# Optimization experiments

Measured on AMD Instinct MI355X. Metric: run time of the kernel, lower is better.

## Reference

```python
import jax, jax.numpy as jnp
import numpy as np

HEADS = 4
DIM_HEAD = 64
SCALE = 8.0
EPS = 1e-5  # fp32 branch of the original LayerNorm


def setup_inputs() -> dict:
    key = jax.random.key(0)
    k1, k2, k3 = jax.random.split(key, 3)
    B, C, F, H, W = 2, 256, 4, 32, 32
    inner = HEADS * DIM_HEAD  # 256
    x = jax.random.normal(k1, (B, C, F, H, W), dtype=jnp.float32)
    gamma = jnp.ones((1, C, 1, 1, 1), dtype=jnp.float32)
    w_qkv = jax.random.normal(k2, (3 * inner, C), dtype=jnp.float32) * 0.05
    w_out = jax.random.normal(k3, (C, inner), dtype=jnp.float32) * 0.05
    return {"x": x, "gamma": gamma, "w_qkv": w_qkv, "w_out": w_out}


def _l2norm(t):
    return t / jnp.sqrt(jnp.sum(t * t, axis=-1, keepdims=True) + 1e-12)


def reference(x, gamma, w_qkv, w_out):
    B, C, F, H, W = x.shape
    N = F * H * W
    inner = HEADS * DIM_HEAD
    residual = x

    # channel LayerNorm (biased variance over dim=1)
    mean = jnp.mean(x, axis=1, keepdims=True)
    var = jnp.mean((x - mean) ** 2, axis=1, keepdims=True)
    xn = (x - mean) / jnp.sqrt(var + EPS) * gamma

    # 1x1x1 conv == channel matmul; flatten spatial dims to sequence
    xn_flat = xn.reshape(B, C, N)                      # [B, C, N]
    qkv = jnp.einsum('oc,bcn->bon', w_qkv, xn_flat)    # [B, 3*inner, N]
    qkv = qkv.reshape(B, 3, HEADS, DIM_HEAD, N)        # chunk then split heads
    qkv = jnp.transpose(qkv, (1, 0, 2, 4, 3))          # [3, B, h, N, d]
    q, k, v = qkv[0], qkv[1], qkv[2]

    q = _l2norm(q)
    k = _l2norm(k)

    sim = jnp.einsum('bhid,bhjd->bhij', q, k) * SCALE  # [B, h, N, N]
    attn = jax.nn.softmax(sim, axis=-1)
    out = jnp.einsum('bhij,bhjd->bhid', attn, v)       # [B, h, N, d]

    # 'b h n d -> b (h d) n' then 1x1x1 out conv
    out = jnp.transpose(out, (0, 1, 3, 2)).reshape(B, inner, N)
    out = jnp.einsum('oi,bin->bon', w_out, out).reshape(B, C, F, H, W)
    return out + residual
```

## Files before the change

### kernel.cpp

```cpp
#include <hip/hip_runtime.h>

#define BATCH 2
#define CCH   256
#define NSEQ  4096
#define NH    4
#define DH    64
#define INNER 256

typedef __attribute__((ext_vector_type(8))) __bf16 bf16x8;
typedef __attribute__((ext_vector_type(4))) float f32x4;
typedef __attribute__((ext_vector_type(8))) unsigned short u16x8;
typedef __attribute__((ext_vector_type(4))) unsigned short u16x4;

#define GLD16(gsrc, ldst)                                                     \
  __builtin_amdgcn_global_load_lds(                                           \
      (const __attribute__((address_space(1))) unsigned int*)(const void*)(gsrc), \
      (__attribute__((address_space(3))) unsigned int*)(void*)(ldst), 16, 0, 0)

static __device__ __forceinline__ unsigned short f2bfr(float f) {
  union { float f; unsigned u; } v; v.f = f;
  return (unsigned short)((v.u + 0x8000u) >> 16);
}
static __device__ __forceinline__ unsigned pack2(float f0, float f1) {
  union { float f; unsigned u; } a, b; a.f = f0; b.f = f1;
  return __builtin_amdgcn_perm(b.u + 0x8000u, a.u + 0x8000u, 0x07060302u);
}
static __device__ __forceinline__ float bf2f(unsigned short u) {
  union { unsigned u; float f; } v; v.u = ((unsigned)u) << 16;
  return v.f;
}
static __device__ __forceinline__ bf16x8 ldb(const unsigned short* p) {
  return *(const bf16x8*)p;
}
static __device__ __forceinline__ f32x4 mm(bf16x8 a, bf16x8 b, f32x4 c) {
  return __builtin_amdgcn_mfma_f32_16x16x32_bf16(a, b, c, 0, 0, 0);
}
static __device__ __forceinline__ float ex2(float x) {
  return __builtin_amdgcn_exp2f(x);
}

__global__ __launch_bounds__(256) void k_lncvt(const float* __restrict__ x,
                                               const float* __restrict__ gamma,
                                               unsigned short* __restrict__ xn,
                                               const float* __restrict__ wq,
                                               const float* __restrict__ wo,
                                               unsigned short* __restrict__ wqb,
                                               unsigned short* __restrict__ wob) {
  int blk = blockIdx.x;
  if (blk >= 256) {
    int t = (blk - 256) * 256 + threadIdx.x;
    int e = t * 4;
    if (e < 768 * 256) {
      float4 v = *(const float4*)(wq + e);
      u16x4 pk = { f2bfr(v.x), f2bfr(v.y), f2bfr(v.z), f2bfr(v.w) };
      *(u16x4*)(wqb + e) = pk;
    } else {
      int e2 = e - 768 * 256;
      float4 v = *(const float4*)(wo + e2);
      u16x4 pk = { f2bfr(v.x), f2bfr(v.y), f2bfr(v.z), f2bfr(v.w) };
      *(u16x4*)(wob + e2) = pk;
    }
    return;
  }
  int b  = blk >> 7;
  int n0 = (blk & 127) * 32;
  int t  = threadIdx.x;
  int nl = t & 31;
  int cg = t >> 5;
  int n  = n0 + nl;
  const float* xp = x + ((size_t)(b * CCH + cg * 32)) * NSEQ + n;
  float vals[32];
  float s = 0.f, s2 = 0.f;
#pragma unroll
  for (int j = 0; j < 32; j++) {
    float v = xp[(size_t)j * NSEQ];
    vals[j] = v; s += v; s2 += v * v;
  }
  __shared__ float rs[8][32], rs2[8][32];
  rs[cg][nl] = s; rs2[cg][nl] = s2;
  __syncthreads();
  float S = 0.f, S2 = 0.f;
#pragma unroll
  for (int g = 0; g < 8; g++) { S += rs[g][nl]; S2 += rs2[g][nl]; }
  float mean = S * (1.f / 256.f);
  float var  = S2 * (1.f / 256.f) - mean * mean;
  float rstd = rsqrtf(var + 1e-5f);
  unsigned short* dst = xn + ((size_t)b * NSEQ + n) * CCH + cg * 32;
#pragma unroll
  for (int j0 = 0; j0 < 32; j0 += 8) {
    u16x8 pk;
#pragma unroll
    for (int j = 0; j < 8; j++)
      pk[j] = f2bfr((vals[j0 + j] - mean) * rstd * gamma[cg * 32 + j0 + j]);
    *(u16x8*)(dst + j0) = pk;
  }
}

__global__ __launch_bounds__(256) void k_qkv(const unsigned short* __restrict__ wqb,
                                             const unsigned short* __restrict__ xn,
                                             unsigned short* __restrict__ qkv,
                                             unsigned short* __restrict__ qt,
                                             unsigned short* __restrict__ ktb) {
  int n0 = blockIdx.x * 64;
  int oi = blockIdx.y;
  int o0 = oi * 64;
  int b  = blockIdx.z;
  __shared__ unsigned short Al[64 * 128];
  __shared__ unsigned short Bl[64 * 128];
  int t = threadIdx.x;
  int lane = t & 63, w = t >> 6;
  int c = lane & 15, quad = lane >> 4;
  int wm = w >> 1, wn = w & 1;
  f32x4 acc[2][2] = {};
  int lr = lane >> 4;
  int lchk = lane & 15;
  const unsigned short* apg = wqb + (size_t)o0 * CCH;
  const unsigned short* bpg = xn + ((size_t)b * NSEQ + n0) * CCH;
  for (int kt = 0; kt < 2; kt++) {
    if (kt) __syncthreads();
#pragma unroll
    for (int q = 0; q < 4; q++) {
      int r = w * 16 + q * 4 + lr;
      int srcoff = r * CCH + kt * 128 + ((lchk ^ (r & 7)) * 8);
      GLD16(apg + srcoff, Al + (size_t)(w * 16 + q * 4) * 128);
      GLD16(bpg + srcoff, Bl + (size_t)(w * 16 + q * 4) * 128);
    }
    __syncthreads();
#pragma unroll
    for (int ks = 0; ks < 4; ks++) {
      int ra0 = wm * 32 + c, ra1 = ra0 + 16;
      int rb0 = wn * 32 + c, rb1 = rb0 + 16;
      bf16x8 a0 = ldb(&Al[ra0 * 128 + (((ks * 4 + quad) ^ (ra0 & 7)) * 8)]);
      bf16x8 a1 = ldb(&Al[ra1 * 128 + (((ks * 4 + quad) ^ (ra1 & 7)) * 8)]);
      bf16x8 b0 = ldb(&Bl[rb0 * 128 + (((ks * 4 + quad) ^ (rb0 & 7)) * 8)]);
      bf16x8 b1 = ldb(&Bl[rb1 * 128 + (((ks * 4 + quad) ^ (rb1 & 7)) * 8)]);
      acc[0][0] = mm(a0, b0, acc[0][0]);
      acc[0][1] = mm(a0, b1, acc[0][1]);
      acc[1][0] = mm(a1, b0, acc[1][0]);
      acc[1][1] = mm(a1, b1, acc[1][1]);
    }
  }
  if (oi < 8) {
    float* sq = (float*)Al;
    float s0 = 0.f, s1 = 0.f;
#pragma unroll
    for (int i = 0; i < 2; i++)
#pragma unroll
      for (int rr = 0; rr < 4; rr++) {
        s0 += acc[i][0][rr] * acc[i][0][rr];
        s1 += acc[i][1][rr] * acc[i][1][rr];
      }
    s0 += __shfl_xor(s0, 16); s0 += __shfl_xor(s0, 32);
    s1 += __shfl_xor(s1, 16); s1 += __shfl_xor(s1, 32);
    __syncthreads();
    if (quad == 0) {
      sq[wm * 64 + wn * 32 + c]      = s0;
      sq[wm * 64 + wn * 32 + 16 + c] = s1;
    }
    __syncthreads();
    float r0 = rsqrtf(sq[wn * 32 + c]      + sq[64 + wn * 32 + c]      + 1e-12f);
    float r1 = rsqrtf(sq[wn * 32 + 16 + c] + sq[64 + wn * 32 + 16 + c] + 1e-12f);
    if (oi < 4) { r0 *= 11.541560327111707f; r1 *= 11.541560327111707f; }
    int h = oi & 3;
    unsigned short* base = (oi < 4 ? qt : ktb) + ((size_t)(b * NH + h) * NSEQ) * DH;
#pragma unroll
    for (int i = 0; i < 2; i++)
#pragma unroll
      for (int j = 0; j < 2; j++) {
        float rsc = j ? r1 : r0;
        int n = n0 + wn * 32 + j * 16 + c;
        int d = wm * 32 + i * 16 + quad * 4;
        uint2 pk = { pack2(acc[i][j][0] * rsc, acc[i][j][1] * rsc),
                     pack2(acc[i][j][2] * rsc, acc[i][j][3] * rsc) };
        *(uint2*)(base + (size_t)n * DH + d) = pk;
      }
  } else {
#pragma unroll
    for (int i = 0; i < 2; i++)
#pragma unroll
      for (int j = 0; j < 2; j++)
#pragma unroll
        for (int rr = 0; rr < 4; rr++) {
          int o = o0 + wm * 32 + i * 16 + quad * 4 + rr;
          int n = n0 + wn * 32 + j * 16 + c;
          qkv[((size_t)b * 768 + o) * NSEQ + n] = f2bfr(acc[i][j][rr]);
        }
  }
}

__global__ __launch_bounds__(256, 4) void k_attn(
    const unsigned short* __restrict__ qt,
    const unsigned short* __restrict__ ktb,
    const unsigned short* __restrict__ qkv,
    unsigned short* __restrict__ opart,
    float* __restrict__ lpart,
    int S, int kvlen) {
  int i0 = blockIdx.x * 128;
  int h  = blockIdx.y;
  int bz = blockIdx.z;
  int b  = bz / S, s = bz % S;
  __shared__ unsigned short Kl[64 * 64];
  __shared__ unsigned short Vl[2][64 * 64];
  __shared__ unsigned short Pl[128 * 64];
  int t = threadIdx.x;
  int lane = t & 63, w = t >> 6;
  int c = lane & 15, quad = lane >> 4;

  const unsigned short* qbase = qt  + ((size_t)(b * NH + h) * NSEQ) * DH;
  const unsigned short* kbase = ktb + ((size_t)(b * NH + h) * NSEQ) * DH;
  const unsigned short* vbase = qkv + ((size_t)b * 768 + 512 + h * 64) * NSEQ;

  int rlo = w * 32 + c, rhi = rlo + 16;
  const unsigned short* qlo = qbase + (size_t)(i0 + rlo) * DH + quad * 8;
  const unsigned short* qhi = qlo + 16 * DH;
  bf16x8 qlo0 = ldb(qlo), qlo1 = ldb(qlo + 32);
  bf16x8 qhi0 = ldb(qhi), qhi1 = ldb(qhi + 32);

  u16x8 onesu;
#pragma unroll
  for (int j = 0; j < 8; j++) onesu[j] = 0x3F80;
  bf16x8 ones = *(bf16x8*)&onesu;

  f32x4 acclo[4] = {}, acchi[4] = {};
  f32x4 accllo = {}, acclhi = {};

  int slr = lane >> 3, slc = lane & 7;
  int ssw = (slc ^ slr) * 8;
  const unsigned short* kp = kbase + (size_t)(s * kvlen + w * 16 + slr) * DH + ssw;
  const unsigned short* vp = vbase + (size_t)(w * 16 + slr) * NSEQ + s * kvlen + ssw;
  int sw0 = (quad ^ (c & 7)) * 8;
  int sw1 = sw0 ^ 32;
  int r7 = rlo & 7;

  int nIt = kvlen / 64;
  GLD16(kp,            &Kl[(w * 16)     * 64]);
  GLD16(kp + 8 * DH,   &Kl[(w * 16 + 8) * 64]);
  GLD16(vp,            &Vl[0][(w * 16)     * 64]);
  GLD16(vp + 8 * NSEQ, &Vl[0][(w * 16 + 8) * 64]);
  kp += 64 * DH; vp += 64;

  for (int it = 0; it < nIt; it++) {
    int cur = it & 1;
    __syncthreads();
    if (it + 1 < nIt) {
      int nb = cur ^ 1;
      GLD16(vp,            &Vl[nb][(w * 16)     * 64]);
      GLD16(vp + 8 * NSEQ, &Vl[nb][(w * 16 + 8) * 64]);
      vp += 64;
    }

#pragma unroll
    for (int jt = 0; jt < 4; jt++) {
      bf16x8 k0 = ldb(&Kl[(jt * 16 + c) * 64 + sw0]);
      bf16x8 k1 = ldb(&Kl[(jt * 16 + c) * 64 + sw1]);
      f32x4 zl = {}; zl = mm(k0, qlo0, zl); zl = mm(k1, qlo1, zl);
      f32x4 zh = {}; zh = mm(k0, qhi0, zh); zh = mm(k1, qhi1, zh);
      int cj = jt * 2 + (quad >> 1);
      int sub = (quad & 1) * 4;
      uint2 pkl = { pack2(ex2(zl[0]), ex2(zl[1])),
                    pack2(ex2(zl[2]), ex2(zl[3])) };
      *(uint2*)&Pl[rlo * 64 + ((cj ^ r7) * 8) + sub] = pkl;
      uint2 pkh = { pack2(ex2(zh[0]), ex2(zh[1])),
                    pack2(ex2(zh[2]), ex2(zh[3])) };
      *(uint2*)&Pl[rhi * 64 + ((cj ^ r7) * 8) + sub] = pkh;
    }
    bf16x8 plo0 = ldb(&Pl[rlo * 64 + ((quad ^ r7) * 8)]);
    bf16x8 plo1 = ldb(&Pl[rlo * 64 + (((quad + 4) ^ r7) * 8)]);
    bf16x8 phi0 = ldb(&Pl[rhi * 64 + ((quad ^ r7) * 8)]);
    bf16x8 phi1 = ldb(&Pl[rhi * 64 + (((quad + 4) ^ r7) * 8)]);

    if (it + 1 < nIt) {
      asm volatile("s_waitcnt lgkmcnt(0)" ::: "memory");
      __builtin_amdgcn_sched_barrier(0);
      __builtin_amdgcn_s_barrier();
      __builtin_amdgcn_sched_barrier(0);
      GLD16(kp,          &Kl[(w * 16)     * 64]);
      GLD16(kp + 8 * DH, &Kl[(w * 16 + 8) * 64]);
      kp += 64 * DH;
    }

#pragma unroll
    for (int dt = 0; dt < 4; dt++) {
      bf16x8 v0 = ldb(&Vl[cur][(dt * 16 + c) * 64 + sw0]);
      bf16x8 v1 = ldb(&Vl[cur][(dt * 16 + c) * 64 + sw1]);
      acclo[dt] = mm(plo0, v0, acclo[dt]);
      acclo[dt] = mm(plo1, v1, acclo[dt]);
      acchi[dt] = mm(phi0, v0, acchi[dt]);
      acchi[dt] = mm(phi1, v1, acchi[dt]);
    }
    accllo = mm(plo0, ones, accllo); accllo = mm(plo1, ones, accllo);
    acclhi = mm(phi0, ones, acclhi); acclhi = mm(phi1, ones, acclhi);
  }

  size_t rb = ((size_t)(b * NH + h) * S + s) * NSEQ + i0 + w * 32;
  if (c == 0) {
#pragma unroll
    for (int rr = 0; rr < 4; rr++) {
      lpart[rb + quad * 4 + rr]      = accllo[rr];
      lpart[rb + 16 + quad * 4 + rr] = acclhi[rr];
    }
  }
#pragma unroll
  for (int rr = 0; rr < 4; rr++)
#pragma unroll
    for (int dt = 0; dt < 4; dt++) {
      opart[(rb + quad * 4 + rr) * 64 + dt * 16 + c]      = f2bfr(acclo[dt][rr]);
      opart[(rb + 16 + quad * 4 + rr) * 64 + dt * 16 + c] = f2bfr(acchi[dt][rr]);
    }
}

__global__ __launch_bounds__(256) void k_merge(
    const unsigned short* __restrict__ opart,
    const float* __restrict__ lpart,
    unsigned short* __restrict__ ao, int S) {
  int t = blockIdx.x * 256 + threadIdx.x;
  int row = t >> 2;
  int dseg = (t & 3) * 16;
  int b = row >> 14, rem = row & 16383;
  int h = rem >> 12, i = rem & 4095;

  float l = 0.f;
  float o[16];
#pragma unroll
  for (int j = 0; j < 16; j++) o[j] = 0.f;
  for (int s = 0; s < S; s++) {
    size_t rb = ((size_t)(b * NH + h) * S + s) * NSEQ + i;
    l += lpart[rb];
    const unsigned short* p = opart + rb * 64 + dseg;
    u16x8 v0 = *(const u16x8*)p;
    u16x8 v1 = *(const u16x8*)(p + 8);
#pragma unroll
    for (int j = 0; j < 8; j++) {
      o[j]     += bf2f(v0[j]);
      o[8 + j] += bf2f(v1[j]);
    }
  }
  float inv = 1.f / l;
  unsigned short* dst = ao + ((size_t)b * NSEQ + i) * INNER + h * 64 + dseg;
  uint4 pk0 = { pack2(o[0] * inv, o[1] * inv),  pack2(o[2] * inv, o[3] * inv),
                pack2(o[4] * inv, o[5] * inv),  pack2(o[6] * inv, o[7] * inv) };
  uint4 pk1 = { pack2(o[8] * inv, o[9] * inv),  pack2(o[10] * inv, o[11] * inv),
                pack2(o[12] * inv, o[13] * inv),pack2(o[14] * inv, o[15] * inv) };
  *(uint4*)dst = pk0;
  *(uint4*)(dst + 8) = pk1;
}

__global__ __launch_bounds__(256) void k_out(const unsigned short* __restrict__ wob,
                                             const unsigned short* __restrict__ ao,
                                             const float* __restrict__ x,
                                             float* __restrict__ out) {
  int n0 = blockIdx.x * 64;
  int o0 = blockIdx.y * 64;
  int b  = blockIdx.z;
  __shared__ unsigned short Al[64 * 128];
  __shared__ unsigned short Bl[64 * 128];
  int t = threadIdx.x;
  int lane = t & 63, w = t >> 6;
  int c = lane & 15, quad = lane >> 4;
  int wm = w >> 1, wn = w & 1;
  f32x4 acc[2][2] = {};
  int lr = lane >> 4;
  int lchk = lane & 15;
  const unsigned short* apg = wob + (size_t)o0 * INNER;
  const unsigned short* bpg = ao + ((size_t)b * NSEQ + n0) * INNER;
  for (int kt = 0; kt < 2; kt++) {
    if (kt) __syncthreads();
#pragma unroll
    for (int q = 0; q < 4; q++) {
      int r = w * 16 + q * 4 + lr;
      int srcoff = r * INNER + kt * 128 + ((lchk ^ (r & 7)) * 8);
      GLD16(apg + srcoff, Al + (size_t)(w * 16 + q * 4) * 128);
      GLD16(bpg + srcoff, Bl + (size_t)(w * 16 + q * 4) * 128);
    }
    __syncthreads();
#pragma unroll
    for (int ks = 0; ks < 4; ks++) {
      int ra0 = wm * 32 + c, ra1 = ra0 + 16;
      int rb0 = wn * 32 + c, rb1 = rb0 + 16;
      bf16x8 a0 = ldb(&Al[ra0 * 128 + (((ks * 4 + quad) ^ (ra0 & 7)) * 8)]);
      bf16x8 a1 = ldb(&Al[ra1 * 128 + (((ks * 4 + quad) ^ (ra1 & 7)) * 8)]);
      bf16x8 b0 = ldb(&Bl[rb0 * 128 + (((ks * 4 + quad) ^ (rb0 & 7)) * 8)]);
      bf16x8 b1 = ldb(&Bl[rb1 * 128 + (((ks * 4 + quad) ^ (rb1 & 7)) * 8)]);
      acc[0][0] = mm(a0, b0, acc[0][0]);
      acc[0][1] = mm(a0, b1, acc[0][1]);
      acc[1][0] = mm(a1, b0, acc[1][0]);
      acc[1][1] = mm(a1, b1, acc[1][1]);
    }
  }
#pragma unroll
  for (int i = 0; i < 2; i++)
#pragma unroll
    for (int j = 0; j < 2; j++)
#pragma unroll
      for (int rr = 0; rr < 4; rr++) {
        int o = o0 + wm * 32 + i * 16 + quad * 4 + rr;
        int n = n0 + wn * 32 + j * 16 + c;
        size_t idx = ((size_t)b * CCH + o) * NSEQ + n;
        out[idx] = acc[i][j][rr] + x[idx];
      }
}

extern "C" void kernel_launch(void* const* d_in, const int* in_sizes, int n_in,
                              void* d_out, int out_size, void* d_ws, size_t ws_size,
                              hipStream_t stream) {
  const float* x     = (const float*)d_in[0];
  const float* gamma = (const float*)d_in[1];
  const float* wq    = (const float*)d_in[2];
  const float* wo    = (const float*)d_in[3];
  float* out = (float*)d_out;

  const size_t MB = 1u << 20;
  char* ws = (char*)d_ws;
  unsigned short* ao  = (unsigned short*)ws;
  unsigned short* xn  = (unsigned short*)(ws + 4 * MB);
  unsigned short* qkv = (unsigned short*)(ws + 8 * MB);
  unsigned short* wqb = (unsigned short*)(ws + 20 * MB);
  unsigned short* wob = (unsigned short*)(ws + 20 * MB + 512 * 1024);
  unsigned short* qt  = (unsigned short*)(ws + 21 * MB);
  unsigned short* ktb = (unsigned short*)(ws + 25 * MB);
  unsigned short* opart = (unsigned short*)(ws + 29 * MB);
  int S;
  if (ws_size >= 48 * MB) S = 4;
  else if (ws_size >= 40 * MB) S = 2;
  else S = 1;
  size_t opart_bytes = (size_t)S * BATCH * NH * NSEQ * DH * 2;
  float* lpart = (float*)(ws + 29 * MB + opart_bytes);
  int kvlen = NSEQ / S;

  k_lncvt<<<dim3(512),          256, 0, stream>>>(x, gamma, xn, wq, wo, wqb, wob);
  k_qkv  <<<dim3(64, 12, 2),    256, 0, stream>>>(wqb, xn, qkv, qt, ktb);
  k_attn <<<dim3(32, 4, 2 * S), 256, 0, stream>>>(qt, ktb, qkv, opart,
                                                  lpart, S, kvlen);
  k_merge<<<dim3(512),          256, 0, stream>>>(opart, lpart, ao, S);
  k_out  <<<dim3(64, 4, 2),     256, 0, stream>>>(wob, ao, x, out);
}
```

Before: 130.0 us.

## Load full K in GEMMs, use hardware bf16 pack, add setprio around MFMAs

The QKV and output projection kernels now stage the whole 256-wide reduction dimension in LDS in one pass, which removes the second load phase and its barrier at the cost of twice the LDS per block (64 KB). In the attention kernel, the manual rounding/perm bf16 packing is replaced with the v_cvt_pk_bf16_f32 instruction. MFMA groups are wrapped in s_setprio to favour matrix issue across waves. An explicit lgkmcnt(0) wait before the barrier is dropped to shorten the stall. Dropping that wait may race on LDS reuse of the K buffer, and the larger LDS footprint lowers occupancy in the GEMMs.

```diff
diff --git a/kernel.cpp b/kernel.cpp
--- a/kernel.cpp
+++ b/kernel.cpp
@@ -24,6 +24,11 @@
 static __device__ __forceinline__ unsigned pack2(float f0, float f1) {
   union { float f; unsigned u; } a, b; a.f = f0; b.f = f1;
   return __builtin_amdgcn_perm(b.u + 0x8000u, a.u + 0x8000u, 0x07060302u);
+}
+static __device__ __forceinline__ unsigned cvtpk(float lo, float hi) {
+  unsigned r;
+  asm("v_cvt_pk_bf16_f32 %0, %1, %2" : "=v"(r) : "v"(lo), "v"(hi));
+  return r;
 }
 static __device__ __forceinline__ float bf2f(unsigned short u) {
   union { unsigned u; float f; } v; v.u = ((unsigned)u) << 16;
@@ -105,40 +110,37 @@
   int oi = blockIdx.y;
   int o0 = oi * 64;
   int b  = blockIdx.z;
-  __shared__ unsigned short Al[64 * 128];
-  __shared__ unsigned short Bl[64 * 128];
+  __shared__ unsigned short Al[64 * 256];
+  __shared__ unsigned short Bl[64 * 256];
   int t = threadIdx.x;
   int lane = t & 63, w = t >> 6;
   int c = lane & 15, quad = lane >> 4;
   int wm = w >> 1, wn = w & 1;
   f32x4 acc[2][2] = {};
-  int lr = lane >> 4;
-  int lchk = lane & 15;
+  int lr2 = lane >> 5;
+  int lch = lane & 31;
   const unsigned short* apg = wqb + (size_t)o0 * CCH;
   const unsigned short* bpg = xn + ((size_t)b * NSEQ + n0) * CCH;
-  for (int kt = 0; kt < 2; kt++) {
-    if (kt) __syncthreads();
-#pragma unroll
-    for (int q = 0; q < 4; q++) {
-      int r = w * 16 + q * 4 + lr;
-      int srcoff = r * CCH + kt * 128 + ((lchk ^ (r & 7)) * 8);
-      GLD16(apg + srcoff, Al + (size_t)(w * 16 + q * 4) * 128);
-      GLD16(bpg + srcoff, Bl + (size_t)(w * 16 + q * 4) * 128);
-    }
-    __syncthreads();
-#pragma unroll
-    for (int ks = 0; ks < 4; ks++) {
-      int ra0 = wm * 32 + c, ra1 = ra0 + 16;
-      int rb0 = wn * 32 + c, rb1 = rb0 + 16;
-      bf16x8 a0 = ldb(&Al[ra0 * 128 + (((ks * 4 + quad) ^ (ra0 & 7)) * 8)]);
-      bf16x8 a1 = ldb(&Al[ra1 * 128 + (((ks * 4 + quad) ^ (ra1 & 7)) * 8)]);
-      bf16x8 b0 = ldb(&Bl[rb0 * 128 + (((ks * 4 + quad) ^ (rb0 & 7)) * 8)]);
-      bf16x8 b1 = ldb(&Bl[rb1 * 128 + (((ks * 4 + quad) ^ (rb1 & 7)) * 8)]);
-      acc[0][0] = mm(a0, b0, acc[0][0]);
-      acc[0][1] = mm(a0, b1, acc[0][1]);
-      acc[1][0] = mm(a1, b0, acc[1][0]);
-      acc[1][1] = mm(a1, b1, acc[1][1]);
-    }
+#pragma unroll
+  for (int q = 0; q < 8; q++) {
+    int r = w * 16 + q * 2 + lr2;
+    int srcoff = r * CCH + ((lch ^ (r & 7)) * 8);
+    GLD16(apg + srcoff, Al + (size_t)(w * 16 + q * 2) * 256);
+    GLD16(bpg + srcoff, Bl + (size_t)(w * 16 + q * 2) * 256);
+  }
+  __syncthreads();
+#pragma unroll
+  for (int ks = 0; ks < 8; ks++) {
+    int ra0 = wm * 32 + c, ra1 = ra0 + 16;
+    int rb0 = wn * 32 + c, rb1 = rb0 + 16;
+    bf16x8 a0 = ldb(&Al[ra0 * 256 + (((ks * 4 + quad) ^ (ra0 & 7)) * 8)]);
+    bf16x8 a1 = ldb(&Al[ra1 * 256 + (((ks * 4 + quad) ^ (ra1 & 7)) * 8)]);
+    bf16x8 b0 = ldb(&Bl[rb0 * 256 + (((ks * 4 + quad) ^ (rb0 & 7)) * 8)]);
+    bf16x8 b1 = ldb(&Bl[rb1 * 256 + (((ks * 4 + quad) ^ (rb1 & 7)) * 8)]);
+    acc[0][0] = mm(a0, b0, acc[0][0]);
+    acc[0][1] = mm(a0, b1, acc[0][1]);
+    acc[1][0] = mm(a1, b0, acc[1][0]);
+    acc[1][1] = mm(a1, b1, acc[1][1]);
   }
   if (oi < 8) {
     float* sq = (float*)Al;
@@ -253,15 +255,17 @@
     for (int jt = 0; jt < 4; jt++) {
       bf16x8 k0 = ldb(&Kl[(jt * 16 + c) * 64 + sw0]);
       bf16x8 k1 = ldb(&Kl[(jt * 16 + c) * 64 + sw1]);
+      __builtin_amdgcn_s_setprio(1);
       f32x4 zl = {}; zl = mm(k0, qlo0, zl); zl = mm(k1, qlo1, zl);
       f32x4 zh = {}; zh = mm(k0, qhi0, zh); zh = mm(k1, qhi1, zh);
+      __builtin_amdgcn_s_setprio(0);
       int cj = jt * 2 + (quad >> 1);
       int sub = (quad & 1) * 4;
-      uint2 pkl = { pack2(ex2(zl[0]), ex2(zl[1])),
-                    pack2(ex2(zl[2]), ex2(zl[3])) };
+      uint2 pkl = { cvtpk(ex2(zl[0]), ex2(zl[1])),
+                    cvtpk(ex2(zl[2]), ex2(zl[3])) };
       *(uint2*)&Pl[rlo * 64 + ((cj ^ r7) * 8) + sub] = pkl;
-      uint2 pkh = { pack2(ex2(zh[0]), ex2(zh[1])),
-                    pack2(ex2(zh[2]), ex2(zh[3])) };
+      uint2 pkh = { cvtpk(ex2(zh[0]), ex2(zh[1])),
+                    cvtpk(ex2(zh[2]), ex2(zh[3])) };
       *(uint2*)&Pl[rhi * 64 + ((cj ^ r7) * 8) + sub] = pkh;
     }
     bf16x8 plo0 = ldb(&Pl[rlo * 64 + ((quad ^ r7) * 8)]);
@@ -270,7 +274,6 @@
     bf16x8 phi1 = ldb(&Pl[rhi * 64 + (((quad + 4) ^ r7) * 8)]);
 
     if (it + 1 < nIt) {
-      asm volatile("s_waitcnt lgkmcnt(0)" ::: "memory");
       __builtin_amdgcn_sched_barrier(0);
       __builtin_amdgcn_s_barrier();
       __builtin_amdgcn_sched_barrier(0);
@@ -283,13 +286,17 @@
     for (int dt = 0; dt < 4; dt++) {
       bf16x8 v0 = ldb(&Vl[cur][(dt * 16 + c) * 64 + sw0]);
       bf16x8 v1 = ldb(&Vl[cur][(dt * 16 + c) * 64 + sw1]);
+      __builtin_amdgcn_s_setprio(1);
       acclo[dt] = mm(plo0, v0, acclo[dt]);
       acclo[dt] = mm(plo1, v1, acclo[dt]);
       acchi[dt] = mm(phi0, v0, acchi[dt]);
       acchi[dt] = mm(phi1, v1, acchi[dt]);
-    }
+      __builtin_amdgcn_s_setprio(0);
+    }
+    __builtin_amdgcn_s_setprio(1);
     accllo = mm(plo0, ones, accllo); accllo = mm(plo1, ones, accllo);
     acclhi = mm(phi0, ones, acclhi); acclhi = mm(phi1, ones, acclhi);
+    __builtin_amdgcn_s_setprio(0);
   }
 
   size_t rb = ((size_t)(b * NH + h) * S + s) * NSEQ + i0 + w * 32;
@@ -352,40 +359,37 @@
   int n0 = blockIdx.x * 64;
   int o0 = blockIdx.y * 64;
   int b  = blockIdx.z;
-  __shared__ unsigned short Al[64 * 128];
-  __shared__ unsigned short Bl[64 * 128];
+  __shared__ unsigned short Al[64 * 256];
+  __shared__ unsigned short Bl[64 * 256];
   int t = threadIdx.x;
   int lane = t & 63, w = t >> 6;
   int c = lane & 15, quad = lane >> 4;
   int wm = w >> 1, wn = w & 1;
   f32x4 acc[2][2] = {};
-  int lr = lane >> 4;
-  int lchk = lane & 15;
+  int lr2 = lane >> 5;
+  int lch = lane & 31;
   const unsigned short* apg = wob + (size_t)o0 * INNER;
   const unsigned short* bpg = ao + ((size_t)b * NSEQ + n0) * INNER;
-  for (int kt = 0; kt < 2; kt++) {
-    if (kt) __syncthreads();
-#pragma unroll
-    for (int q = 0; q < 4; q++) {
-      int r = w * 16 + q * 4 + lr;
-      int srcoff = r * INNER + kt * 128 + ((lchk ^ (r & 7)) * 8);
-      GLD16(apg + srcoff, Al + (size_t)(w * 16 + q * 4) * 128);
-      GLD16(bpg + srcoff, Bl + (size_t)(w * 16 + q * 4) * 128);
-    }
-    __syncthreads();
-#pragma unroll
-    for (int ks = 0; ks < 4; ks++) {
-      int ra0 = wm * 32 + c, ra1 = ra0 + 16;
-      int rb0 = wn * 32 + c, rb1 = rb0 + 16;
-      bf16x8 a0 = ldb(&Al[ra0 * 128 + (((ks * 4 + quad) ^ (ra0 & 7)) * 8)]);
-      bf16x8 a1 = ldb(&Al[ra1 * 128 + (((ks * 4 + quad) ^ (ra1 & 7)) * 8)]);
-      bf16x8 b0 = ldb(&Bl[rb0 * 128 + (((ks * 4 + quad) ^ (rb0 & 7)) * 8)]);
-      bf16x8 b1 = ldb(&Bl[rb1 * 128 + (((ks * 4 + quad) ^ (rb1 & 7)) * 8)]);
-      acc[0][0] = mm(a0, b0, acc[0][0]);
-      acc[0][1] = mm(a0, b1, acc[0][1]);
-      acc[1][0] = mm(a1, b0, acc[1][0]);
-      acc[1][1] = mm(a1, b1, acc[1][1]);
-    }
+#pragma unroll
+  for (int q = 0; q < 8; q++) {
+    int r = w * 16 + q * 2 + lr2;
+    int srcoff = r * INNER + ((lch ^ (r & 7)) * 8);
+    GLD16(apg + srcoff, Al + (size_t)(w * 16 + q * 2) * 256);
+    GLD16(bpg + srcoff, Bl + (size_t)(w * 16 + q * 2) * 256);
+  }
+  __syncthreads();
+#pragma unroll
+  for (int ks = 0; ks < 8; ks++) {
+    int ra0 = wm * 32 + c, ra1 = ra0 + 16;
+    int rb0 = wn * 32 + c, rb1 = rb0 + 16;
+    bf16x8 a0 = ldb(&Al[ra0 * 256 + (((ks * 4 + quad) ^ (ra0 & 7)) * 8)]);
+    bf16x8 a1 = ldb(&Al[ra1 * 256 + (((ks * 4 + quad) ^ (ra1 & 7)) * 8)]);
+    bf16x8 b0 = ldb(&Bl[rb0 * 256 + (((ks * 4 + quad) ^ (rb0 & 7)) * 8)]);
+    bf16x8 b1 = ldb(&Bl[rb1 * 256 + (((ks * 4 + quad) ^ (rb1 & 7)) * 8)]);
+    acc[0][0] = mm(a0, b0, acc[0][0]);
+    acc[0][1] = mm(a0, b1, acc[0][1]);
+    acc[1][0] = mm(a1, b0, acc[1][0]);
+    acc[1][1] = mm(a1, b1, acc[1][1]);
   }
 #pragma unroll
   for (int i = 0; i < 2; i++)
```

Measured after the change: 128.9 us. Within noise of the previous version (-0.9%).
